# Performance work log

Measured on AMD Instinct MI355X. Metric: run time of the kernel, lower is better.

Reference implementation:

```python
import jax, jax.numpy as jnp
import numpy as np

NUM_CODES = 8192
DIM = 8
BETA = 0.25
TAU = 1.0
EPS = 1e-10


def setup_inputs() -> dict:
    key = jax.random.key(0)
    k1, k2, k3 = jax.random.split(key, 3)
    z_e = jax.random.normal(k1, (8, DIM, 32, 32), dtype=jnp.float32)
    embedding = jax.random.normal(k2, (NUM_CODES, DIM), dtype=jnp.float32) * 0.01
    proj_w = jax.random.normal(k3, (NUM_CODES, DIM), dtype=jnp.float32) * (1.0 / np.sqrt(DIM))
    return {"z_e": z_e, "embedding": embedding, "proj_w": proj_w}


def reference(z_e, embedding, proj_w):
    B, D, H, W = z_e.shape
    K = embedding.shape[0]
    # (B, D, H, W) -> (N, D), N = B*H*W  (matches permute(0,2,3,1).reshape(-1,d))
    z_flat = jnp.transpose(z_e, (0, 2, 3, 1)).reshape(-1, D)
    # 1x1 conv == matmul against (K, D) weight
    logits = z_flat @ proj_w.T  # (N, K)  -- dominant memory traffic
    # Gumbel-softmax with hard=True (training path), fixed noise key
    u = jax.random.uniform(jax.random.key(42), logits.shape,
                           dtype=logits.dtype, minval=1e-20, maxval=1.0)
    gumbel = -jnp.log(-jnp.log(u))
    y_soft = jax.nn.softmax((logits + gumbel) / TAU, axis=-1)
    idx = jnp.argmax(y_soft, axis=-1)  # (N,)
    y_hard = jax.nn.one_hot(idx, K, dtype=y_soft.dtype)
    # straight-through: forward = hard one-hot, backward = soft
    st = y_hard + y_soft - jax.lax.stop_gradient(y_soft)
    z_q_flat = st @ embedding  # (N, D) -- effectively a gather in forward
    z_q = jnp.transpose(z_q_flat.reshape(B, H, W, D), (0, 3, 1, 2))
    # commitment loss against detached re-lookup
    q_flat = jax.lax.stop_gradient(embedding[idx])
    commit_loss = BETA * jnp.mean((z_flat - q_flat) ** 2)
    # usage stats (no-grad in original)
    counts = jnp.zeros((K,), z_e.dtype).at[idx].add(1.0)
    avg = counts / idx.shape[0]
    perplexity = jnp.exp(-jnp.sum(avg * jnp.log(avg + EPS)))
    usage = jnp.sum(counts > 0).astype(z_e.dtype) / K
    indices = idx.reshape(B, H, W)
    return z_q, indices, commit_loss, perplexity, usage
```

## Files before the change

kernel.cpp:

```cpp
#include <hip/hip_runtime.h>
#include <stdint.h>


#define NCODES 8192
#define NROWS  8192

__device__ int g_hist[NCODES];


#define TF4_R1 \
  "v_mov_b32 %4, %8\n" "v_mov_b32 %5, %9\n" \
  "v_mov_b32 %6, %10\n" "v_mov_b32 %7, %11\n" \
  "v_alignbit_b32 %0, %8, %8, 19\n" "v_alignbit_b32 %1, %9, %9, 19\n" \
  "v_alignbit_b32 %2, %10, %10, 19\n" "v_alignbit_b32 %3, %11, %11, 19\n" \
  "v_xor_b32 %0, %0, %4\n" "v_xor_b32 %1, %1, %5\n" \
  "v_xor_b32 %2, %2, %6\n" "v_xor_b32 %3, %3, %7\n"

#define TF4_ADD \
  "v_add_u32 %4, %4, %0\n" "v_add_u32 %5, %5, %1\n" \
  "v_add_u32 %6, %6, %2\n" "v_add_u32 %7, %7, %3\n"

#define TF4_ADD3_42 \
  "v_add3_u32 %4, %4, %0, 42\n" "v_add3_u32 %5, %5, %1, 42\n" \
  "v_add3_u32 %6, %6, %2, 42\n" "v_add3_u32 %7, %7, %3, 42\n"

#define TF4_ROT(s) \
  "v_alignbit_b32 %0, %0, %0, " #s "\n" "v_alignbit_b32 %1, %1, %1, " #s "\n" \
  "v_alignbit_b32 %2, %2, %2, " #s "\n" "v_alignbit_b32 %3, %3, %3, " #s "\n"

#define TF4_XOR \
  "v_xor_b32 %0, %0, %4\n" "v_xor_b32 %1, %1, %5\n" \
  "v_xor_b32 %2, %2, %6\n" "v_xor_b32 %3, %3, %7\n"

#define TF4_AX1(lit) \
  "v_add_u32 %0, " #lit ", %0\n" "v_add_u32 %1, " #lit ", %1\n" \
  "v_add_u32 %2, " #lit ", %2\n" "v_add_u32 %3, " #lit ", %3\n"

#define TF4_AX0(lit) \
  "v_add_u32 %4, " #lit ", %4\n" "v_add_u32 %5, " #lit ", %5\n" \
  "v_add_u32 %6, " #lit ", %6\n" "v_add_u32 %7, " #lit ", %7\n"

#define TF4_RN(s)  TF4_ADD     TF4_ROT(s) TF4_XOR
#define TF4_RN3(s) TF4_ADD3_42 TF4_ROT(s) TF4_XOR

#define GVQ_C   0.36651292058166435f
#define GVQ_LN2 0.69314718055994530942f
__device__ __forceinline__ float gvq17_gumbel(uint32_t bits) {
    float u = __uint_as_float((bits >> 9) | 0x3f800000u) - 1.0f;
    float l1 = __builtin_amdgcn_logf(u);
    float l2 = __builtin_amdgcn_logf(0.0f - l1);
    return fmaf(-GVQ_LN2, l2, GVQ_C);
}

__global__ __launch_bounds__(1024) void gvq17_init(float* out) {
    const int t = threadIdx.x;
    for (int k = t; k < NCODES; k += 1024) g_hist[k] = 0;
    if (t == 0) out[73728] = 0.0f;
}

#define DOT8(zz) \
    fmaf(zz[7], wb.w, fmaf(zz[6], wb.z, fmaf(zz[5], wb.y, fmaf(zz[4], wb.x, \
    fmaf(zz[3], wa.w, fmaf(zz[2], wa.z, fmaf(zz[1], wa.y, zz[0] * wa.x)))))))

__global__ __launch_bounds__(256, 5) void gvq17_argmax(const float* __restrict__ z_e,
                                                       const float* __restrict__ proj_w,
                                                       const float* __restrict__ emb,
                                                       float* __restrict__ out) {
    __shared__ float sv[4][256];
    __shared__ int   sj[4][256];
    __shared__ float ssq[4];
    const int tid = threadIdx.x;
    const int n0 = blockIdx.x * 4;

    float z0[8], z1[8], z2[8], z3[8];
    {
        const int b = n0 >> 10, r = n0 & 1023;
        (void)b; (void)r;
    }
#pragma unroll
    for (int d = 0; d < 8; ++d) {
        const int nA = n0 + 0, nB = n0 + 1, nC = n0 + 2, nD = n0 + 3;
        z0[d] = z_e[(nA >> 10) * 8192 + d * 1024 + (nA & 1023)];
        z1[d] = z_e[(nB >> 10) * 8192 + d * 1024 + (nB & 1023)];
        z2[d] = z_e[(nC >> 10) * 8192 + d * 1024 + (nC & 1023)];
        z3[d] = z_e[(nD >> 10) * 8192 + d * 1024 + (nD & 1023)];
    }

    uint32_t ca = ((uint32_t)(n0 + 0) << 13) + (uint32_t)tid + 42u;
    uint32_t cb = ((uint32_t)(n0 + 1) << 13) + (uint32_t)tid + 42u;
    uint32_t cc = ((uint32_t)(n0 + 2) << 13) + (uint32_t)tid + 42u;
    uint32_t cd = ((uint32_t)(n0 + 3) << 13) + (uint32_t)tid + 42u;

    const float4* p = ((const float4*)proj_w) + 2 * tid;
    float best0 = -INFINITY, best1 = -INFINITY, best2 = -INFINITY, best3 = -INFINITY;
    int bi0 = 0, bi1 = 0, bi2 = 0, bi3 = 0;
    int k = tid;

    for (int i = 0; i < 32; ++i) {
        float4 wa = p[0];
        float4 wb = p[1];
        p += 512;

        float d0 = DOT8(z0);
        float d1 = DOT8(z1);
        float d2 = DOT8(z2);
        float d3 = DOT8(z3);

        uint32_t o0, o1, o2, o3, t0, t1, t2, t3;
        asm(TF4_R1
            TF4_RN(17) TF4_RN(6) TF4_RN(26)
            TF4_AX1(0x1BD11BF1)
            TF4_RN3(15) TF4_RN(3) TF4_RN(16) TF4_RN(8)
            TF4_AX0(0x1BD11BF0) TF4_AX1(2)
            TF4_RN(19) TF4_RN(17) TF4_RN(6) TF4_RN(26)
            TF4_AX1(45)
            TF4_RN(15) TF4_RN(3) TF4_RN(16) TF4_RN(8)
            TF4_AX1(0x1BD11BF4)
            TF4_RN3(19) TF4_RN(17) TF4_RN(6) TF4_RN(26)
            TF4_AX0(0x1BD11BF0) TF4_AX1(5)
            TF4_XOR
            : "=&v"(o0), "=&v"(o1), "=&v"(o2), "=&v"(o3),
              "=&v"(t0), "=&v"(t1), "=&v"(t2), "=&v"(t3)
            : "v"(ca), "v"(cb), "v"(cc), "v"(cd));
        (void)t0; (void)t1; (void)t2; (void)t3;

        float v0 = d0 + gvq17_gumbel(o0);
        float v1 = d1 + gvq17_gumbel(o1);
        float v2 = d2 + gvq17_gumbel(o2);
        float v3 = d3 + gvq17_gumbel(o3);

        if (v0 > best0) { best0 = v0; bi0 = k; }
        if (v1 > best1) { best1 = v1; bi1 = k; }
        if (v2 > best2) { best2 = v2; bi2 = k; }
        if (v3 > best3) { best3 = v3; bi3 = k; }

        ca += 256u; cb += 256u; cc += 256u; cd += 256u;
        k += 256;
    }

    sv[0][tid] = best0; sj[0][tid] = bi0;
    sv[1][tid] = best1; sj[1][tid] = bi1;
    sv[2][tid] = best2; sj[2][tid] = bi2;
    sv[3][tid] = best3; sj[3][tid] = bi3;
    __syncthreads();
    for (int s = 128; s > 0; s >>= 1) {
        if (tid < s) {
#pragma unroll
            for (int r = 0; r < 4; ++r) {
                float va = sv[r][tid + s];
                if (va > sv[r][tid] ||
                    (va == sv[r][tid] && sj[r][tid + s] < sj[r][tid])) {
                    sv[r][tid] = va; sj[r][tid] = sj[r][tid + s];
                }
            }
        }
        __syncthreads();
    }

    if (tid < 4) {
        const int n = n0 + tid;
        const int idx = sj[tid][0];
        out[65536 + n] = (float)idx;
        atomicAdd(&g_hist[idx], 1);
        float zz[8];
#pragma unroll
        for (int d = 0; d < 8; ++d) {
            zz[d] = (tid == 0) ? z0[d] : (tid == 1) ? z1[d]
                  : (tid == 2) ? z2[d] : z3[d];
        }
        const float4* ep = (const float4*)(emb + idx * 8);
        float4 ea = ep[0], eb = ep[1];
        float e[8] = {ea.x, ea.y, ea.z, ea.w, eb.x, eb.y, eb.z, eb.w};
        const int b = n >> 10, r = n & 1023;
        float sq = 0.0f;
#pragma unroll
        for (int d = 0; d < 8; ++d) {
            out[b * 8192 + d * 1024 + r] = e[d];
            float diff = zz[d] - e[d];
            sq = fmaf(diff, diff, sq);
        }
        ssq[tid] = sq;
    }
    __syncthreads();
    if (tid == 0)
        atomicAdd(out + 73728, ssq[0] + ssq[1] + ssq[2] + ssq[3]);
}

__global__ __launch_bounds__(1024) void gvq17_stats(float* __restrict__ out) {
    __shared__ float hred[1024];
    __shared__ int   ired[1024];
    const int tid = threadIdx.x;

    float h = 0.0f; int used = 0;
    for (int kk = tid; kk < NCODES; kk += 1024) {
        int c = g_hist[kk];
        float avg = (float)c * (1.0f / 8192.0f);
        h += avg * logf(avg + 1e-10f);
        used += (c > 0) ? 1 : 0;
    }
    hred[tid] = h; ired[tid] = used;
    __syncthreads();
    for (int t = 512; t > 0; t >>= 1) {
        if (tid < t) { hred[tid] += hred[tid + t]; ired[tid] += ired[tid + t]; }
        __syncthreads();
    }
    if (tid == 0) {
        float accum = out[73728];
        out[73728] = 0.25f * accum * (1.0f / 65536.0f);
        out[73729] = expf(-hred[0]);
        out[73730] = (float)ired[0] * (1.0f / 8192.0f);
    }
}

extern "C" void kernel_launch(void* const* d_in, const int* in_sizes, int n_in,
                              void* d_out, int out_size, void* d_ws, size_t ws_size,
                              hipStream_t stream) {
    const float* z_e   = (const float*)d_in[0];
    const float* emb   = (const float*)d_in[1];
    const float* projw = (const float*)d_in[2];
    float* out = (float*)d_out;

    gvq17_init  <<<1,    1024, 0, stream>>>(out);
    gvq17_argmax<<<2048, 256,  0, stream>>>(z_e, projw, emb, out);
    gvq17_stats <<<1,    1024, 0, stream>>>(out);
}
```

Before: 212.4 us.

## Halve rows per block, fold stats into last-block epilogue, widen init

```diff
diff --git a/kernel.cpp b/kernel.cpp
--- a/kernel.cpp
+++ b/kernel.cpp
@@ -6,6 +6,7 @@
 #define NROWS  8192
 
 __device__ int g_hist[NCODES];
+__device__ int g_done;
 
 
 #define TF4_R1 \
@@ -45,66 +46,63 @@
 
 #define GVQ_C   0.36651292058166435f
 #define GVQ_LN2 0.69314718055994530942f
-__device__ __forceinline__ float gvq17_gumbel(uint32_t bits) {
-    float u = __uint_as_float((bits >> 9) | 0x3f800000u) - 1.0f;
+__device__ __forceinline__ float gvq18_gumbel(uint32_t bits) {
+    float u = __uint_as_float(__builtin_amdgcn_alignbit(0x7Fu, bits, 9u)) - 1.0f;
     float l1 = __builtin_amdgcn_logf(u);
-    float l2 = __builtin_amdgcn_logf(0.0f - l1);
+    float l2 = __builtin_amdgcn_logf(-l1);
     return fmaf(-GVQ_LN2, l2, GVQ_C);
 }
 
-__global__ __launch_bounds__(1024) void gvq17_init(float* out) {
-    const int t = threadIdx.x;
-    for (int k = t; k < NCODES; k += 1024) g_hist[k] = 0;
-    if (t == 0) out[73728] = 0.0f;
-}
-
-#define DOT8(zz) \
+__global__ __launch_bounds__(256) void gvq18_init(float* out) {
+    const int k = blockIdx.x * 256 + threadIdx.x;
+    g_hist[k] = 0;
+    if (k == 0) { out[73728] = 0.0f; g_done = 0; }
+}
+
+#define DOT8(zz, wa, wb) \
     fmaf(zz[7], wb.w, fmaf(zz[6], wb.z, fmaf(zz[5], wb.y, fmaf(zz[4], wb.x, \
     fmaf(zz[3], wa.w, fmaf(zz[2], wa.z, fmaf(zz[1], wa.y, zz[0] * wa.x)))))))
 
-__global__ __launch_bounds__(256, 5) void gvq17_argmax(const float* __restrict__ z_e,
+__global__ __launch_bounds__(256, 5) void gvq18_argmax(const float* __restrict__ z_e,
                                                        const float* __restrict__ proj_w,
                                                        const float* __restrict__ emb,
                                                        float* __restrict__ out) {
-    __shared__ float sv[4][256];
-    __shared__ int   sj[4][256];
-    __shared__ float ssq[4];
+    __shared__ float sv[2][256];
+    __shared__ int   sj[2][256];
+    __shared__ float ssq[2];
+    __shared__ int   is_last;
     const int tid = threadIdx.x;
-    const int n0 = blockIdx.x * 4;
-
-    float z0[8], z1[8], z2[8], z3[8];
-    {
-        const int b = n0 >> 10, r = n0 & 1023;
-        (void)b; (void)r;
-    }
+    const int n0 = blockIdx.x * 2;
+    const int n1 = n0 + 1;
+
+    float z0[8], z1[8];
 #pragma unroll
     for (int d = 0; d < 8; ++d) {
-        const int nA = n0 + 0, nB = n0 + 1, nC = n0 + 2, nD = n0 + 3;
-        z0[d] = z_e[(nA >> 10) * 8192 + d * 1024 + (nA & 1023)];
-        z1[d] = z_e[(nB >> 10) * 8192 + d * 1024 + (nB & 1023)];
-        z2[d] = z_e[(nC >> 10) * 8192 + d * 1024 + (nC & 1023)];
-        z3[d] = z_e[(nD >> 10) * 8192 + d * 1024 + (nD & 1023)];
-    }
-
-    uint32_t ca = ((uint32_t)(n0 + 0) << 13) + (uint32_t)tid + 42u;
-    uint32_t cb = ((uint32_t)(n0 + 1) << 13) + (uint32_t)tid + 42u;
-    uint32_t cc = ((uint32_t)(n0 + 2) << 13) + (uint32_t)tid + 42u;
-    uint32_t cd = ((uint32_t)(n0 + 3) << 13) + (uint32_t)tid + 42u;
-
-    const float4* p = ((const float4*)proj_w) + 2 * tid;
-    float best0 = -INFINITY, best1 = -INFINITY, best2 = -INFINITY, best3 = -INFINITY;
-    int bi0 = 0, bi1 = 0, bi2 = 0, bi3 = 0;
+        z0[d] = z_e[(n0 >> 10) * 8192 + d * 1024 + (n0 & 1023)];
+        z1[d] = z_e[(n1 >> 10) * 8192 + d * 1024 + (n1 & 1023)];
+    }
+
+    uint32_t ca = ((uint32_t)n0 << 13) + (uint32_t)tid + 42u;
+    uint32_t cb = ca + 256u;
+    uint32_t cc = ca + 8192u;
+    uint32_t cd = ca + 8448u;
+
+    const float4* wr = (const float4*)proj_w;
+    float bA0 = -INFINITY, bB0 = -INFINITY, bA1 = -INFINITY, bB1 = -INFINITY;
+    int iA0 = 0, iB0 = 0, iA1 = 0, iB1 = 0;
     int k = tid;
 
-    for (int i = 0; i < 32; ++i) {
-        float4 wa = p[0];
-        float4 wb = p[1];
-        p += 512;
-
-        float d0 = DOT8(z0);
-        float d1 = DOT8(z1);
-        float d2 = DOT8(z2);
-        float d3 = DOT8(z3);
+    for (int i = 0; i < 16; ++i) {
+        const int base = (i << 10) + 2 * tid;
+        float4 wa0 = wr[base];
+        float4 wb0 = wr[base + 1];
+        float4 wa1 = wr[base + 512];
+        float4 wb1 = wr[base + 513];
+
+        float dA0 = DOT8(z0, wa0, wb0);
+        float dB0 = DOT8(z0, wa1, wb1);
+        float dA1 = DOT8(z1, wa0, wb0);
+        float dB1 = DOT8(z1, wa1, wb1);
 
         uint32_t o0, o1, o2, o3, t0, t1, t2, t3;
         asm(TF4_R1
@@ -124,50 +122,50 @@
             : "v"(ca), "v"(cb), "v"(cc), "v"(cd));
         (void)t0; (void)t1; (void)t2; (void)t3;
 
-        float v0 = d0 + gvq17_gumbel(o0);
-        float v1 = d1 + gvq17_gumbel(o1);
-        float v2 = d2 + gvq17_gumbel(o2);
-        float v3 = d3 + gvq17_gumbel(o3);
-
-        if (v0 > best0) { best0 = v0; bi0 = k; }
-        if (v1 > best1) { best1 = v1; bi1 = k; }
-        if (v2 > best2) { best2 = v2; bi2 = k; }
-        if (v3 > best3) { best3 = v3; bi3 = k; }
-
-        ca += 256u; cb += 256u; cc += 256u; cd += 256u;
-        k += 256;
-    }
+        float vA0 = dA0 + gvq18_gumbel(o0);
+        float vB0 = dB0 + gvq18_gumbel(o1);
+        float vA1 = dA1 + gvq18_gumbel(o2);
+        float vB1 = dB1 + gvq18_gumbel(o3);
+
+        if (vA0 > bA0) { bA0 = vA0; iA0 = k; }
+        if (vB0 > bB0) { bB0 = vB0; iB0 = k + 256; }
+        if (vA1 > bA1) { bA1 = vA1; iA1 = k; }
+        if (vB1 > bB1) { bB1 = vB1; iB1 = k + 256; }
+
+        ca += 512u; cb += 512u; cc += 512u; cd += 512u;
+        k += 512;
+    }
+
+    float best0 = bA0; int bi0 = iA0;
+    if (bB0 > best0 || (bB0 == best0 && iB0 < bi0)) { best0 = bB0; bi0 = iB0; }
+    float best1 = bA1; int bi1 = iA1;
+    if (bB1 > best1 || (bB1 == best1 && iB1 < bi1)) { best1 = bB1; bi1 = iB1; }
 
     sv[0][tid] = best0; sj[0][tid] = bi0;
     sv[1][tid] = best1; sj[1][tid] = bi1;
-    sv[2][tid] = best2; sj[2][tid] = bi2;
-    sv[3][tid] = best3; sj[3][tid] = bi3;
     __syncthreads();
     for (int s = 128; s > 0; s >>= 1) {
         if (tid < s) {
 #pragma unroll
-            for (int r = 0; r < 4; ++r) {
+            for (int r = 0; r < 2; ++r) {
                 float va = sv[r][tid + s];
-                if (va > sv[r][tid] ||
-                    (va == sv[r][tid] && sj[r][tid + s] < sj[r][tid])) {
-                    sv[r][tid] = va; sj[r][tid] = sj[r][tid + s];
+                int   ja = sj[r][tid + s];
+                if (va > sv[r][tid] || (va == sv[r][tid] && ja < sj[r][tid])) {
+                    sv[r][tid] = va; sj[r][tid] = ja;
                 }
             }
         }
         __syncthreads();
     }
 
-    if (tid < 4) {
+    if (tid < 2) {
         const int n = n0 + tid;
         const int idx = sj[tid][0];
         out[65536 + n] = (float)idx;
         atomicAdd(&g_hist[idx], 1);
         float zz[8];
 #pragma unroll
-        for (int d = 0; d < 8; ++d) {
-            zz[d] = (tid == 0) ? z0[d] : (tid == 1) ? z1[d]
-                  : (tid == 2) ? z2[d] : z3[d];
-        }
+        for (int d = 0; d < 8; ++d) zz[d] = (tid == 0) ? z0[d] : z1[d];
         const float4* ep = (const float4*)(emb + idx * 8);
         float4 ea = ep[0], eb = ep[1];
         float e[8] = {ea.x, ea.y, ea.z, ea.w, eb.x, eb.y, eb.z, eb.w};
@@ -182,33 +180,37 @@
         ssq[tid] = sq;
     }
     __syncthreads();
-    if (tid == 0)
-        atomicAdd(out + 73728, ssq[0] + ssq[1] + ssq[2] + ssq[3]);
-}
-
-__global__ __launch_bounds__(1024) void gvq17_stats(float* __restrict__ out) {
-    __shared__ float hred[1024];
-    __shared__ int   ired[1024];
-    const int tid = threadIdx.x;
-
-    float h = 0.0f; int used = 0;
-    for (int kk = tid; kk < NCODES; kk += 1024) {
-        int c = g_hist[kk];
-        float avg = (float)c * (1.0f / 8192.0f);
-        h += avg * logf(avg + 1e-10f);
-        used += (c > 0) ? 1 : 0;
-    }
-    hred[tid] = h; ired[tid] = used;
+    if (tid == 0) {
+        atomicAdd(out + 73728, ssq[0] + ssq[1]);
+        __threadfence();
+        int old = __hip_atomic_fetch_add(&g_done, 1, __ATOMIC_ACQ_REL,
+                                         __HIP_MEMORY_SCOPE_AGENT);
+        is_last = (old == 4095);
+    }
     __syncthreads();
-    for (int t = 512; t > 0; t >>= 1) {
-        if (tid < t) { hred[tid] += hred[tid + t]; ired[tid] += ired[tid + t]; }
+
+    if (is_last) {
+        float h = 0.0f; int used = 0;
+        for (int kk = tid; kk < NCODES; kk += 256) {
+            int c = __hip_atomic_load(&g_hist[kk], __ATOMIC_RELAXED,
+                                      __HIP_MEMORY_SCOPE_AGENT);
+            float avg = (float)c * (1.0f / 8192.0f);
+            h += avg * logf(avg + 1e-10f);
+            used += (c > 0) ? 1 : 0;
+        }
+        sv[0][tid] = h; sj[0][tid] = used;
         __syncthreads();
-    }
-    if (tid == 0) {
-        float accum = out[73728];
-        out[73728] = 0.25f * accum * (1.0f / 65536.0f);
-        out[73729] = expf(-hred[0]);
-        out[73730] = (float)ired[0] * (1.0f / 8192.0f);
+        for (int s = 128; s > 0; s >>= 1) {
+            if (tid < s) { sv[0][tid] += sv[0][tid + s]; sj[0][tid] += sj[0][tid + s]; }
+            __syncthreads();
+        }
+        if (tid == 0) {
+            float accum = __hip_atomic_load(out + 73728, __ATOMIC_RELAXED,
+                                            __HIP_MEMORY_SCOPE_AGENT);
+            out[73728] = 0.25f * accum * (1.0f / 65536.0f);
+            out[73729] = expf(-sv[0][0]);
+            out[73730] = (float)sj[0][0] * (1.0f / 8192.0f);
+        }
     }
 }
 
@@ -220,7 +222,6 @@
     const float* projw = (const float*)d_in[2];
     float* out = (float*)d_out;
 
-    gvq17_init  <<<1,    1024, 0, stream>>>(out);
-    gvq17_argmax<<<2048, 256,  0, stream>>>(z_e, projw, emb, out);
-    gvq17_stats <<<1,    1024, 0, stream>>>(out);
-}
+    gvq18_init  <<<32,   256, 0, stream>>>(out);
+    gvq18_argmax<<<4096, 256, 0, stream>>>(z_e, projw, emb, out);
+}
```

Result: slower. 301.8 us (+42.1%).

## Fuse init and stats kernels into argmax via last-block completion counter

Applied to the files above, without the earlier changes.

```diff
diff --git a/kernel.cpp b/kernel.cpp
--- a/kernel.cpp
+++ b/kernel.cpp
@@ -4,8 +4,11 @@
 
 #define NCODES 8192
 #define NROWS  8192
-
-__device__ int g_hist[NCODES];
+#define NBLOCKS 2048
+
+__device__ int   g_hist[NCODES];
+__device__ int   g_done;
+__device__ float g_commit;
 
 
 #define TF4_R1 \
@@ -45,38 +48,29 @@
 
 #define GVQ_C   0.36651292058166435f
 #define GVQ_LN2 0.69314718055994530942f
-__device__ __forceinline__ float gvq17_gumbel(uint32_t bits) {
-    float u = __uint_as_float((bits >> 9) | 0x3f800000u) - 1.0f;
+__device__ __forceinline__ float gvq19_gumbel(uint32_t bits) {
+    float u = __uint_as_float(__builtin_amdgcn_alignbit(0x7Fu, bits, 9u)) - 1.0f;
     float l1 = __builtin_amdgcn_logf(u);
-    float l2 = __builtin_amdgcn_logf(0.0f - l1);
+    float l2 = __builtin_amdgcn_logf(-l1);
     return fmaf(-GVQ_LN2, l2, GVQ_C);
-}
-
-__global__ __launch_bounds__(1024) void gvq17_init(float* out) {
-    const int t = threadIdx.x;
-    for (int k = t; k < NCODES; k += 1024) g_hist[k] = 0;
-    if (t == 0) out[73728] = 0.0f;
 }
 
 #define DOT8(zz) \
     fmaf(zz[7], wb.w, fmaf(zz[6], wb.z, fmaf(zz[5], wb.y, fmaf(zz[4], wb.x, \
     fmaf(zz[3], wa.w, fmaf(zz[2], wa.z, fmaf(zz[1], wa.y, zz[0] * wa.x)))))))
 
-__global__ __launch_bounds__(256, 5) void gvq17_argmax(const float* __restrict__ z_e,
+__global__ __launch_bounds__(256, 4) void gvq19_argmax(const float* __restrict__ z_e,
                                                        const float* __restrict__ proj_w,
                                                        const float* __restrict__ emb,
                                                        float* __restrict__ out) {
     __shared__ float sv[4][256];
     __shared__ int   sj[4][256];
     __shared__ float ssq[4];
+    __shared__ int   is_last;
     const int tid = threadIdx.x;
     const int n0 = blockIdx.x * 4;
 
     float z0[8], z1[8], z2[8], z3[8];
-    {
-        const int b = n0 >> 10, r = n0 & 1023;
-        (void)b; (void)r;
-    }
 #pragma unroll
     for (int d = 0; d < 8; ++d) {
         const int nA = n0 + 0, nB = n0 + 1, nC = n0 + 2, nD = n0 + 3;
@@ -124,10 +118,10 @@
             : "v"(ca), "v"(cb), "v"(cc), "v"(cd));
         (void)t0; (void)t1; (void)t2; (void)t3;
 
-        float v0 = d0 + gvq17_gumbel(o0);
-        float v1 = d1 + gvq17_gumbel(o1);
-        float v2 = d2 + gvq17_gumbel(o2);
-        float v3 = d3 + gvq17_gumbel(o3);
+        float v0 = d0 + gvq19_gumbel(o0);
+        float v1 = d1 + gvq19_gumbel(o1);
+        float v2 = d2 + gvq19_gumbel(o2);
+        float v3 = d3 + gvq19_gumbel(o3);
 
         if (v0 > best0) { best0 = v0; bi0 = k; }
         if (v1 > best1) { best1 = v1; bi1 = k; }
@@ -148,9 +142,9 @@
 #pragma unroll
             for (int r = 0; r < 4; ++r) {
                 float va = sv[r][tid + s];
-                if (va > sv[r][tid] ||
-                    (va == sv[r][tid] && sj[r][tid + s] < sj[r][tid])) {
-                    sv[r][tid] = va; sj[r][tid] = sj[r][tid + s];
+                int   ja = sj[r][tid + s];
+                if (va > sv[r][tid] || (va == sv[r][tid] && ja < sj[r][tid])) {
+                    sv[r][tid] = va; sj[r][tid] = ja;
                 }
             }
         }
@@ -182,33 +176,40 @@
         ssq[tid] = sq;
     }
     __syncthreads();
-    if (tid == 0)
-        atomicAdd(out + 73728, ssq[0] + ssq[1] + ssq[2] + ssq[3]);
-}
-
-__global__ __launch_bounds__(1024) void gvq17_stats(float* __restrict__ out) {
-    __shared__ float hred[1024];
-    __shared__ int   ired[1024];
-    const int tid = threadIdx.x;
-
-    float h = 0.0f; int used = 0;
-    for (int kk = tid; kk < NCODES; kk += 1024) {
-        int c = g_hist[kk];
-        float avg = (float)c * (1.0f / 8192.0f);
-        h += avg * logf(avg + 1e-10f);
-        used += (c > 0) ? 1 : 0;
-    }
-    hred[tid] = h; ired[tid] = used;
+    if (tid == 0) {
+        atomicAdd(&g_commit, ssq[0] + ssq[1] + ssq[2] + ssq[3]);
+        __threadfence();
+        int old = __hip_atomic_fetch_add(&g_done, 1, __ATOMIC_ACQ_REL,
+                                         __HIP_MEMORY_SCOPE_AGENT);
+        is_last = (old == NBLOCKS - 1);
+    }
     __syncthreads();
-    for (int t = 512; t > 0; t >>= 1) {
-        if (tid < t) { hred[tid] += hred[tid + t]; ired[tid] += ired[tid + t]; }
+
+    if (is_last) {
+        float h = 0.0f; int used = 0;
+        for (int kk = tid; kk < NCODES; kk += 256) {
+            int c = __hip_atomic_load(&g_hist[kk], __ATOMIC_RELAXED,
+                                      __HIP_MEMORY_SCOPE_AGENT);
+            float avg = (float)c * (1.0f / 8192.0f);
+            h += avg * logf(avg + 1e-10f);
+            used += (c > 0) ? 1 : 0;
+            g_hist[kk] = 0;
+        }
+        sv[0][tid] = h; sj[0][tid] = used;
         __syncthreads();
-    }
-    if (tid == 0) {
-        float accum = out[73728];
-        out[73728] = 0.25f * accum * (1.0f / 65536.0f);
-        out[73729] = expf(-hred[0]);
-        out[73730] = (float)ired[0] * (1.0f / 8192.0f);
+        for (int s = 128; s > 0; s >>= 1) {
+            if (tid < s) { sv[0][tid] += sv[0][tid + s]; sj[0][tid] += sj[0][tid + s]; }
+            __syncthreads();
+        }
+        if (tid == 0) {
+            float accum = __hip_atomic_load(&g_commit, __ATOMIC_RELAXED,
+                                            __HIP_MEMORY_SCOPE_AGENT);
+            out[73728] = 0.25f * accum * (1.0f / 65536.0f);
+            out[73729] = expf(-sv[0][0]);
+            out[73730] = (float)sj[0][0] * (1.0f / 8192.0f);
+            g_commit = 0.0f;
+            g_done = 0;
+        }
     }
 }
 
@@ -220,7 +221,5 @@
     const float* projw = (const float*)d_in[2];
     float* out = (float*)d_out;
 
-    gvq17_init  <<<1,    1024, 0, stream>>>(out);
-    gvq17_argmax<<<2048, 256,  0, stream>>>(z_e, projw, emb, out);
-    gvq17_stats <<<1,    1024, 0, stream>>>(out);
+    gvq19_argmax<<<NBLOCKS, 256, 0, stream>>>(z_e, projw, emb, out);
 }
```

Measured after the change: 249.7 us. 17.6% more time.
